# Kernel tuning notes

Hardware: AMD Instinct MI355X
Metric: run time of the kernel (lower is better)

## Reference

```python
import jax, jax.numpy as jnp
import numpy as np

ARRAY_SIZE = 128   # crossbar rows
CBITS = 4          # psum ADC bits
LEV = 2 ** (CBITS - 1)
ALPHA = ARRAY_SIZE / LEV   # psum quant step
EPS = 1e-5

# ---- binary activation / weight quant with STE (hardtanh grad) ----
@jax.custom_vjp
def ste_sign(x):
    return jnp.where(x >= 0, 1.0, -1.0).astype(x.dtype)

def _sign_fwd(x):
    return ste_sign(x), x

def _sign_bwd(x, g):
    return (g * (jnp.abs(x) <= 1.0).astype(g.dtype),)

ste_sign.defvjp(_sign_fwd, _sign_bwd)

# ---- psum (partial-sum) quantization: cbits-level ADC over each crossbar array ----
@jax.custom_vjp
def psum_quant(p):
    return jnp.clip(jnp.round(p / ALPHA), -LEV, LEV - 1) * ALPHA

def _pq_fwd(p):
    return psum_quant(p), p

def _pq_bwd(p, g):
    return (g * (jnp.abs(p) <= ARRAY_SIZE).astype(g.dtype),)

psum_quant.defvjp(_pq_fwd, _pq_bwd)

# ---- layers ----
def bn(x, p):
    g, b, m, v = p  # each [C]
    sh = (1, -1) + (1,) * (x.ndim - 2)
    return (x - m.reshape(sh)) * (g.reshape(sh) / jnp.sqrt(v.reshape(sh) + EPS)) + b.reshape(sh)

def maxpool2(x):
    return jax.lax.reduce_window(x, -jnp.inf, jax.lax.max, (1, 1, 2, 2), (1, 1, 2, 2), 'VALID')

def conv_same(x, w):
    return jax.lax.conv_general_dilated(x, w, (1, 1), 'SAME')

def psum_conv(x, w):
    # crossbar-mapped conv: input channels split into groups of arraySize//(kh*kw),
    # each group conv'd separately, psum-quantized (ADC), then accumulated.
    O, Cin, kh, kw = w.shape
    chunk = max(1, ARRAY_SIZE // (kh * kw))
    G = -(-Cin // chunk)
    pad = G * chunk - Cin
    xp = jnp.pad(x, ((0, 0), (0, pad), (0, 0), (0, 0)))
    wp = jnp.pad(w, ((0, 0), (0, pad), (0, 0), (0, 0)))
    B, _, H, W = x.shape
    xg = xp.reshape(B, G, chunk, H, W).transpose(1, 0, 2, 3, 4)   # [G,B,c,H,W]
    wg = wp.reshape(O, G, chunk, kh, kw).transpose(1, 0, 2, 3, 4)  # [G,O,c,kh,kw]
    ps = jax.vmap(conv_same)(xg, wg)                               # [G,B,O,H,W]
    return psum_quant(ps).sum(0)

def psum_linear(x, w):
    # x [B,D], w [O,D]; D divisible by ARRAY_SIZE
    B, D = x.shape
    O = w.shape[0]
    G = D // ARRAY_SIZE
    ps = jnp.einsum('bgc,ogc->gbo', x.reshape(B, G, ARRAY_SIZE), w.reshape(O, G, ARRAY_SIZE))
    return psum_quant(ps).sum(0)


def setup_inputs() -> dict:
    key = jax.random.key(0)
    ks = iter(jax.random.split(key, 64))
    def nrm(shape, s=0.05):
        return jax.random.normal(next(ks), shape, jnp.float32) * s
    def bnp(C):
        return jnp.stack([jax.random.uniform(next(ks), (C,), jnp.float32) + 0.5,
                          nrm((C,), 0.1), nrm((C,), 0.1),
                          jax.random.uniform(next(ks), (C,), jnp.float32) + 0.5])
    return dict(
        x=jax.random.normal(next(ks), (64, 3, 32, 32), jnp.float32),
        conv0_w=nrm((128, 3, 3, 3)), bn0=bnp(128),
        w1=nrm((128, 128, 3, 3)), bn1=bnp(128),
        w2=nrm((256, 128, 3, 3)), bn2=bnp(256),
        w3=nrm((256, 256, 3, 3)), bn3=bnp(256),
        w4=nrm((512, 256, 3, 3)), bn4=bnp(512),
        w5=nrm((512, 512, 3, 3)), bn5=bnp(512),
        fc1_w=nrm((1024, 8192)), bnf1=bnp(1024),
        fc2_w=nrm((1024, 1024)), bnf2=bnp(1024),
        out_w=nrm((10, 1024)), out_b=nrm((10,)), bnout=bnp(10),
    )


def reference(x, conv0_w, bn0, w1, bn1, w2, bn2, w3, bn3, w4, bn4, w5, bn5,
              fc1_w, bnf1, fc2_w, bnf2, out_w, out_b, bnout):
    h = conv_same(x, conv0_w)                       # full-precision first conv
    h = ste_sign(bn(h, bn0))
    h = psum_conv(h, ste_sign(w1)); h = maxpool2(h); h = ste_sign(bn(h, bn1))
    h = psum_conv(h, ste_sign(w2)); h = ste_sign(bn(h, bn2))
    h = psum_conv(h, ste_sign(w3)); h = maxpool2(h); h = ste_sign(bn(h, bn3))
    h = psum_conv(h, ste_sign(w4)); h = ste_sign(bn(h, bn4))
    h = psum_conv(h, ste_sign(w5)); h = maxpool2(h); h = ste_sign(bn(h, bn5))
    h = h.reshape(h.shape[0], -1)                   # [B, 8192]
    h = ste_sign(bn(psum_linear(h, ste_sign(fc1_w)), bnf1))
    h = bn(psum_linear(h, ste_sign(fc2_w)), bnf2)   # abits=32 -> identity nonlinear
    h = h @ out_w.T + out_b
    return bn(h, bnout)
```

## Files before the change

### kernel.cpp

```cpp
#include <hip/hip_runtime.h>
#include <cstdint>
#include <cstddef>

using bf16x8 = __attribute__((ext_vector_type(8))) short;
using f32x4  = __attribute__((ext_vector_type(4))) float;
using u32x4  = __attribute__((ext_vector_type(4))) unsigned int;

#define DI __device__ __forceinline__

DI float pq3(float a) {
    return fminf(rintf(a), 7.f);
}
DI float pq16(float ps) {
    return fminf(rintf(ps * 0.0625f), 7.f) * 16.f;
}

DI float bnv(float x, float g, float b, float m, float v) {
    return (x - m) * (g / sqrtf(v + 1e-5f)) + b;
}

DI unsigned short sgn_bf16(float v) {
    return (v >= 0.f) ? (unsigned short)0x3F80 : (unsigned short)0xBF80;
}

__global__ __launch_bounds__(256)
void k_conv0(const float* __restrict__ x, const float* __restrict__ w,
             const float* __restrict__ bnp, unsigned short* __restrict__ out) {
    __shared__ float sX[3][3][36];
    const int b = blockIdx.x >> 5, y = blockIdx.x & 31;
    const int tid = threadIdx.x;
    const int o = tid & 127, xc = tid >> 7;

    for (int i = tid; i < 3 * 3 * 36; i += 256) {
        int col = i % 36, rr = (i / 36) % 3, c = i / 108;
        int gy = y + rr - 1, gx = col - 1;
        float v = 0.f;
        if ((unsigned)gy < 32u && (unsigned)gx < 32u)
            v = x[((b * 3 + c) * 32 + gy) * 32 + gx];
        sX[c][rr][col] = v;
    }
    float wr[27];
    const float* wp = w + o * 27;
    #pragma unroll
    for (int t = 0; t < 27; ++t) wr[t] = wp[t];
    __syncthreads();

    const float bg = bnp[o], bb = bnp[128 + o], bm = bnp[256 + o], bv = bnp[384 + o];
    unsigned short* op = out + ((size_t)(b * 32 + y) * 32) * 128 + o;

    #pragma unroll
    for (int q = 0; q < 4; ++q) {
        float acc0 = 0.f, acc1 = 0.f, acc2 = 0.f, acc3 = 0.f;
        const int X0 = xc * 16 + q * 4;
        #pragma unroll
        for (int c = 0; c < 3; ++c)
            #pragma unroll
            for (int ky = 0; ky < 3; ++ky) {
                float xv0 = sX[c][ky][X0 + 0], xv1 = sX[c][ky][X0 + 1];
                float xv2 = sX[c][ky][X0 + 2], xv3 = sX[c][ky][X0 + 3];
                float xv4 = sX[c][ky][X0 + 4], xv5 = sX[c][ky][X0 + 5];
                float w0 = wr[c * 9 + ky * 3 + 0];
                float w1 = wr[c * 9 + ky * 3 + 1];
                float w2 = wr[c * 9 + ky * 3 + 2];
                acc0 += xv0 * w0 + xv1 * w1 + xv2 * w2;
                acc1 += xv1 * w0 + xv2 * w1 + xv3 * w2;
                acc2 += xv2 * w0 + xv3 * w1 + xv4 * w2;
                acc3 += xv3 * w0 + xv4 * w1 + xv5 * w2;
            }
        op[(size_t)(X0 + 0) * 128] = sgn_bf16(bnv(acc0, bg, bb, bm, bv));
        op[(size_t)(X0 + 1) * 128] = sgn_bf16(bnv(acc1, bg, bb, bm, bv));
        op[(size_t)(X0 + 2) * 128] = sgn_bf16(bnv(acc2, bg, bb, bm, bv));
        op[(size_t)(X0 + 3) * 128] = sgn_bf16(bnv(acc3, bg, bb, bm, bv));
    }
}

__global__ __launch_bounds__(256)
void k_pack_w2(const float* __restrict__ w, unsigned short* __restrict__ wpk,
               int Cin, int O, int G) {
    int idx = blockIdx.x * 256 + threadIdx.x;
    if (idx >= G * O * 160) return;
    int c8 = idx & 7;
    int o  = (idx >> 3) % O;
    int r2 = (idx >> 3) / O;
    int chdw = r2 & 1, tap = (r2 >> 1) % 10, g = r2 / 20;
    int c = chdw * 8 + c8, cg = g * 14 + c;
    unsigned short v = 0;
    if (tap < 9 && c < 14 && cg < Cin)
        v = (w[((size_t)o * Cin + cg) * 9 + tap] >= 0.f) ? (unsigned short)0x3D80
                                                         : (unsigned short)0xBD80;
    wpk[idx] = v;
}

template <int H, int W, int Cin, int O, int G, int RH, int RW, int POOLMODE>
__global__ __launch_bounds__(256)
void k_conv_mfma(const unsigned int* __restrict__ act,
                 const char* __restrict__ wpk2,
                 const float* __restrict__ bnp,
                 unsigned short* __restrict__ outa,
                 unsigned short* __restrict__ a5p,
                 const unsigned int* __restrict__ zbuf) {
    constexpr int SH = RH + 2, SW = RW + 2;
    constexpr int MS = RH * RW / 16;
    constexpr int NREGX = W / RW;
    constexpr int SLOT8 = SH * SW * 8;
    constexpr int NST = (SLOT8 + 255) / 256;
    static_assert(MS == 4, "2x2 decomposition needs MS==4");
    static_assert(POOLMODE != 1 || RW == 16, "pool mode 1 needs RW=16");
    static_assert(POOLMODE != 2 || RW == 8, "pool mode 2 needs 8x8");

    __shared__ __align__(16) unsigned int sA[SH * SW * 12];

    const int tid  = threadIdx.x;
    const int regY = (int)blockIdx.x / NREGX, regX = (int)blockIdx.x % NREGX;
    const int o0   = blockIdx.y * 64;
    const int b    = blockIdx.z;

    const int lane = tid & 63, wv = tid >> 6;
    const int n  = lane & 15;
    const int kb = lane >> 4;
    const int hb = kb >> 1, ch = kb & 1;
    const int mp = wv & 1;
    const int oh = wv >> 1;

    const unsigned int* sptr[NST];
    int sdst[NST];
    #pragma unroll
    for (int it = 0; it < NST; ++it) {
        int i = it * 256 + tid;
        sdst[it] = -1;
        if (i < SLOT8) {
            int cp = i & 7, slot = i >> 3;
            int yy = slot / SW, xx = slot - yy * SW;
            int gy = regY * RH + yy - 1, gx = regX * RW + xx - 1;
            sdst[it] = slot * 12 + (((cp >> 2) + slot) % 3) * 4 + (cp & 3);
            sptr[it] = ((unsigned)gy < (unsigned)H && (unsigned)gx < (unsigned)W)
                     ? act + ((size_t)(b * H + gy) * W + gx) * (Cin / 2) + cp
                     : zbuf + cp;
        }
    }

    int offMS[2][5];
    #pragma unroll
    for (int j = 0; j < 2; ++j) {
        int p = (2 * mp + j) * 16 + n;
        int y = p / RW, x = p % RW;
        #pragma unroll
        for (int s = 0; s < 5; ++s) {
            int t = 2 * s + hb;
            int slotT = (t <= 8) ? ((y + t / 3) * SW + (x + t % 3)) : (y * SW + x);
            offMS[j][s] = slotT * 48 + ((ch + slotT) % 3) * 16;
        }
    }

    float tot[2][2][4];
    #pragma unroll
    for (int j = 0; j < 2; ++j)
        #pragma unroll
        for (int hf = 0; hf < 2; ++hf)
            #pragma unroll
            for (int r = 0; r < 4; ++r) tot[j][hf][r] = 0.f;

    const char* wl = wpk2 + (size_t)(o0 + oh * 32 + n) * 16 + (size_t)ch * (O * 16);

    #pragma unroll 1
    for (int g = 0; g < G; ++g) {
        #pragma unroll
        for (int it = 0; it < NST; ++it)
            if (sdst[it] >= 0) {
                sA[sdst[it]] = *sptr[it];
                sptr[it] += 7;
            }
        bf16x8 bq[2][5];
        #pragma unroll
        for (int s = 0; s < 5; ++s) {
            const char* wt = wl + (size_t)(2 * s + hb) * (2 * O * 16);
            bq[0][s] = *(const bf16x8*)(wt);
            bq[1][s] = *(const bf16x8*)(wt + 256);
        }
        wl += (size_t)20 * O * 16;
        __syncthreads();

        const char* sAc = (const char*)sA;
        #pragma unroll
        for (int j = 0; j < 2; ++j) {
            f32x4 a0 = {0.f, 0.f, 0.f, 0.f}, a1 = {0.f, 0.f, 0.f, 0.f};
            #pragma unroll
            for (int s = 0; s < 5; ++s) {
                bf16x8 af = *(const bf16x8*)(sAc + offMS[j][s]);
                a0 = __builtin_amdgcn_mfma_f32_16x16x32_bf16(af, bq[0][s], a0, 0, 0, 0);
                a1 = __builtin_amdgcn_mfma_f32_16x16x32_bf16(af, bq[1][s], a1, 0, 0, 0);
            }
            #pragma unroll
            for (int r = 0; r < 4; ++r) {
                tot[j][0][r] += pq3(a0[r]);
                tot[j][1][r] += pq3(a1[r]);
            }
        }
        __syncthreads();
    }

    #pragma unroll
    for (int hf = 0; hf < 2; ++hf) {
        const int oc = o0 + oh * 32 + hf * 16 + n;
        const float bg = bnp[oc], bb = bnp[O + oc], bm = bnp[2 * O + oc], bvr = bnp[3 * O + oc];

        if constexpr (POOLMODE == 0) {
            #pragma unroll
            for (int j = 0; j < 2; ++j)
                #pragma unroll
                for (int r = 0; r < 4; ++r) {
                    int p = (2 * mp + j) * 16 + 4 * kb + r;
                    int y = regY * RH + p / RW, x = regX * RW + p % RW;
                    float val = bnv(16.f * tot[j][hf][r], bg, bb, bm, bvr);
                    outa[(((size_t)b * H + y) * W + x) * O + oc] = sgn_bf16(val);
                }
        } else if constexpr (POOLMODE == 1) {
            #pragma unroll
            for (int q = 0; q < 2; ++q) {
                float v = fmaxf(fmaxf(tot[0][hf][2 * q], tot[0][hf][2 * q + 1]),
                                fmaxf(tot[1][hf][2 * q], tot[1][hf][2 * q + 1]));
                float val = bnv(16.f * v, bg, bb, bm, bvr);
                int py = regY * (RH / 2) + mp, px = regX * (RW / 2) + 2 * kb + q;
                outa[(((size_t)b * (H / 2) + py) * (W / 2) + px) * O + oc] = sgn_bf16(val);
            }
        } else {
            #pragma unroll
            for (int j = 0; j < 2; ++j)
                #pragma unroll
                for (int q = 0; q < 2; ++q) {
                    float h = fmaxf(tot[j][hf][2 * q], tot[j][hf][2 * q + 1]);
                    float o2 = __shfl_xor(h, 32);
                    float v = fmaxf(h, o2);
                    if (hb == 0) {
                        float val = bnv(16.f * v, bg, bb, bm, bvr);
                        int d = oc * 16 + (2 * mp + j) * 4 + 2 * ch + q;
                        a5p[((size_t)(d >> 3) * 64 + b) * 8 + (d & 7)] = sgn_bf16(val);
                    }
                }
        }
    }
}

template <int D, int GPB>
__global__ __launch_bounds__(256)
void k_fc_mfma(const unsigned short* __restrict__ bpk, const float* __restrict__ w,
               float* __restrict__ accg) {
    const int lane = threadIdx.x & 63, wv = threadIdx.x >> 6;
    const int n = lane & 15, kb = lane >> 4;
    const int orow = blockIdx.x * 64 + wv * 16 + n;
    const int g0 = blockIdx.y * GPB;

    float tot[4][4];
    #pragma unroll
    for (int s = 0; s < 4; ++s)
        #pragma unroll
        for (int r = 0; r < 4; ++r) tot[s][r] = 0.f;

    #pragma unroll 1
    for (int g = 0; g < GPB; ++g) {
        const int kbase = (g0 + g) * 128;
        f32x4 a0 = {0,0,0,0}, a1 = {0,0,0,0}, a2 = {0,0,0,0}, a3 = {0,0,0,0};
        #pragma unroll
        for (int s = 0; s < 4; ++s) {
            const int k0 = kbase + s * 32 + kb * 8;
            const float* wp = w + (size_t)orow * D + k0;
            float4 wlo = *(const float4*)wp;
            float4 whi = *(const float4*)(wp + 4);
            bf16x8 af;
            af[0] = (short)sgn_bf16(wlo.x); af[1] = (short)sgn_bf16(wlo.y);
            af[2] = (short)sgn_bf16(wlo.z); af[3] = (short)sgn_bf16(wlo.w);
            af[4] = (short)sgn_bf16(whi.x); af[5] = (short)sgn_bf16(whi.y);
            af[6] = (short)sgn_bf16(whi.z); af[7] = (short)sgn_bf16(whi.w);
            const unsigned short* bp = bpk + (size_t)(k0 >> 3) * 512;
            bf16x8 b0 = *(const bf16x8*)(bp + (n +  0) * 8);
            bf16x8 b1 = *(const bf16x8*)(bp + (n + 16) * 8);
            bf16x8 b2 = *(const bf16x8*)(bp + (n + 32) * 8);
            bf16x8 b3 = *(const bf16x8*)(bp + (n + 48) * 8);
            a0 = __builtin_amdgcn_mfma_f32_16x16x32_bf16(af, b0, a0, 0, 0, 0);
            a1 = __builtin_amdgcn_mfma_f32_16x16x32_bf16(af, b1, a1, 0, 0, 0);
            a2 = __builtin_amdgcn_mfma_f32_16x16x32_bf16(af, b2, a2, 0, 0, 0);
            a3 = __builtin_amdgcn_mfma_f32_16x16x32_bf16(af, b3, a3, 0, 0, 0);
        }
        #pragma unroll
        for (int r = 0; r < 4; ++r) {
            tot[0][r] += pq16(a0[r]); tot[1][r] += pq16(a1[r]);
            tot[2][r] += pq16(a2[r]); tot[3][r] += pq16(a3[r]);
        }
    }
    const int od = blockIdx.x * 64 + wv * 16 + kb * 4;
    #pragma unroll
    for (int s = 0; s < 4; ++s)
        #pragma unroll
        for (int r = 0; r < 4; ++r)
            atomicAdd(&accg[(size_t)(od + r) * 64 + s * 16 + n], tot[s][r]);
}

template <bool SIGN>
__global__ __launch_bounds__(256)
void k_fc_ep(const float* __restrict__ accg, const float* __restrict__ bnp,
             unsigned short* __restrict__ packed, float* __restrict__ h2, int O) {
    int idx = blockIdx.x * 256 + threadIdx.x;
    int b = idx & 63, o = idx >> 6;
    float val = bnv(accg[idx], bnp[o], bnp[O + o], bnp[2 * O + o], bnp[3 * O + o]);
    if (SIGN) packed[((size_t)(o >> 3) * 64 + b) * 8 + (o & 7)] = sgn_bf16(val);
    else      h2[(size_t)b * 1024 + o] = val;
}

__global__ __launch_bounds__(64)
void k_out(const float* __restrict__ h2, const float* __restrict__ ow,
           const float* __restrict__ ob, const float* __restrict__ bnp,
           float* __restrict__ out) {
    int b = blockIdx.x / 10, o = blockIdx.x % 10;
    int lane = threadIdx.x;
    float acc = 0.f;
    #pragma unroll
    for (int i = 0; i < 16; ++i) {
        int k = i * 64 + lane;
        acc += h2[b * 1024 + k] * ow[o * 1024 + k];
    }
    #pragma unroll
    for (int off = 32; off; off >>= 1) acc += __shfl_xor(acc, off);
    if (lane == 0)
        out[b * 10 + o] = bnv(acc + ob[o], bnp[o], bnp[10 + o], bnp[20 + o], bnp[30 + o]);
}

extern "C" void kernel_launch(void* const* d_in, const int* in_sizes, int n_in,
                              void* d_out, int out_size, void* d_ws, size_t ws_size,
                              hipStream_t stream) {
    const float* x     = (const float*)d_in[0];
    const float* w0    = (const float*)d_in[1];
    const float* bn0   = (const float*)d_in[2];
    const float* w1    = (const float*)d_in[3];
    const float* bn1   = (const float*)d_in[4];
    const float* w2    = (const float*)d_in[5];
    const float* bn2   = (const float*)d_in[6];
    const float* w3    = (const float*)d_in[7];
    const float* bn3   = (const float*)d_in[8];
    const float* w4    = (const float*)d_in[9];
    const float* bn4   = (const float*)d_in[10];
    const float* w5    = (const float*)d_in[11];
    const float* bn5   = (const float*)d_in[12];
    const float* fc1w  = (const float*)d_in[13];
    const float* bnf1  = (const float*)d_in[14];
    const float* fc2w  = (const float*)d_in[15];
    const float* bnf2  = (const float*)d_in[16];
    const float* outw  = (const float*)d_in[17];
    const float* outb  = (const float*)d_in[18];
    const float* bnout = (const float*)d_in[19];

    char* ws = (char*)d_ws;
    unsigned short* actA  = (unsigned short*)(ws);
    unsigned short* actB  = (unsigned short*)(ws + 16777216);
    unsigned short* wpk   = (unsigned short*)(ws + 20971520);
    unsigned short* a5p   = (unsigned short*)(ws + 27262976);
    unsigned short* a6p   = (unsigned short*)(ws + 28311552);
    float*          h1acc = (float*)(ws + 28442624);
    float*          h2acc = (float*)(ws + 28704768);
    float*          h2    = (float*)(ws + 28966912);
    unsigned int*   zbuf  = (unsigned int*)(ws + 29229056);

    const unsigned int* actA32 = (const unsigned int*)actA;
    const unsigned int* actB32 = (const unsigned int*)actB;
    const char* wpkc = (const char*)wpk;

    hipMemsetAsync(h1acc, 0, 262144, stream);
    hipMemsetAsync(h2acc, 0, 262144, stream);
    hipMemsetAsync(zbuf, 0, 4096, stream);

    k_conv0<<<dim3(2048), dim3(256), 0, stream>>>(x, w0, bn0, actA);

    k_pack_w2<<<dim3(800), dim3(256), 0, stream>>>(w1, wpk, 128, 128, 10);
    k_conv_mfma<32, 32, 128, 128, 10, 4, 16, 1>
        <<<dim3(16, 2, 64), dim3(256), 0, stream>>>(actA32, wpkc, bn1, actB, nullptr, zbuf);

    k_pack_w2<<<dim3(1600), dim3(256), 0, stream>>>(w2, wpk, 128, 256, 10);
    k_conv_mfma<16, 16, 128, 256, 10, 4, 16, 0>
        <<<dim3(4, 4, 64), dim3(256), 0, stream>>>(actB32, wpkc, bn2, actA, nullptr, zbuf);

    k_pack_w2<<<dim3(3040), dim3(256), 0, stream>>>(w3, wpk, 256, 256, 19);
    k_conv_mfma<16, 16, 256, 256, 19, 4, 16, 1>
        <<<dim3(4, 4, 64), dim3(256), 0, stream>>>(actA32, wpkc, bn3, actB, nullptr, zbuf);

    k_pack_w2<<<dim3(6080), dim3(256), 0, stream>>>(w4, wpk, 256, 512, 19);
    k_conv_mfma<8, 8, 256, 512, 19, 8, 8, 0>
        <<<dim3(1, 8, 64), dim3(256), 0, stream>>>(actB32, wpkc, bn4, actA, nullptr, zbuf);

    k_pack_w2<<<dim3(11840), dim3(256), 0, stream>>>(w5, wpk, 512, 512, 37);
    k_conv_mfma<8, 8, 512, 512, 37, 8, 8, 2>
        <<<dim3(1, 8, 64), dim3(256), 0, stream>>>(actA32, wpkc, bn5, nullptr, a5p, zbuf);

    k_fc_mfma<8192, 1><<<dim3(16, 64), dim3(256), 0, stream>>>(a5p, fc1w, h1acc);
    k_fc_ep<true><<<dim3(256), dim3(256), 0, stream>>>(h1acc, bnf1, a6p, nullptr, 1024);
    k_fc_mfma<1024, 1><<<dim3(16, 8), dim3(256), 0, stream>>>(a6p, fc2w, h2acc);
    k_fc_ep<false><<<dim3(256), dim3(256), 0, stream>>>(h2acc, bnf2, nullptr, h2, 1024);
    k_out<<<dim3(640), dim3(64), 0, stream>>>(h2, outw, outb, bnout, (float*)d_out);
}
```

Baseline: 269.2 us.

## Switch crossbar conv MFMA from 16x16x32 to 32x32x16 tiles with tap-wise K

Rewrites the binary conv inner loop so each wave computes a 32-pixel by 32-channel tile with 32x32x16 bf16 MFMAs, one per 3x3 tap, instead of pairs of 16x16x32 MFMAs over packed tap pairs. This drops the padding tenth tap, so there are fewer MFMA slots per group. Weight fragments are now loaded inside the compute loop rather than before the barrier. The epilogue is remapped to the 32x32 accumulator layout for the plain, 2x2-pool and flattened-pool output modes. The risk is higher accumulator register pressure and longer MFMA latency chains, which two alternating accumulators only partly hide.

```diff
diff --git a/kernel.cpp b/kernel.cpp
--- a/kernel.cpp
+++ b/kernel.cpp
@@ -4,6 +4,7 @@
 
 using bf16x8 = __attribute__((ext_vector_type(8))) short;
 using f32x4  = __attribute__((ext_vector_type(4))) float;
+using f32x16 = __attribute__((ext_vector_type(16))) float;
 using u32x4  = __attribute__((ext_vector_type(4))) unsigned int;
 
 #define DI __device__ __forceinline__
@@ -100,11 +101,10 @@
                  unsigned short* __restrict__ a5p,
                  const unsigned int* __restrict__ zbuf) {
     constexpr int SH = RH + 2, SW = RW + 2;
-    constexpr int MS = RH * RW / 16;
     constexpr int NREGX = W / RW;
     constexpr int SLOT8 = SH * SW * 8;
     constexpr int NST = (SLOT8 + 255) / 256;
-    static_assert(MS == 4, "2x2 decomposition needs MS==4");
+    static_assert(RH * RW == 64, "tile must be 64 px");
     static_assert(POOLMODE != 1 || RW == 16, "pool mode 1 needs RW=16");
     static_assert(POOLMODE != 2 || RW == 8, "pool mode 2 needs 8x8");
 
@@ -116,11 +116,10 @@
     const int b    = blockIdx.z;
 
     const int lane = tid & 63, wv = tid >> 6;
-    const int n  = lane & 15;
-    const int kb = lane >> 4;
-    const int hb = kb >> 1, ch = kb & 1;
-    const int mp = wv & 1;
-    const int oh = wv >> 1;
+    const int ph   = wv & 1;
+    const int ohl  = wv >> 1;
+    const int l31  = lane & 31;
+    const int chdw = lane >> 5;
 
     const unsigned int* sptr[NST];
     int sdst[NST];
@@ -139,28 +138,19 @@
         }
     }
 
-    int offMS[2][5];
-    #pragma unroll
-    for (int j = 0; j < 2; ++j) {
-        int p = (2 * mp + j) * 16 + n;
-        int y = p / RW, x = p % RW;
-        #pragma unroll
-        for (int s = 0; s < 5; ++s) {
-            int t = 2 * s + hb;
-            int slotT = (t <= 8) ? ((y + t / 3) * SW + (x + t % 3)) : (y * SW + x);
-            offMS[j][s] = slotT * 48 + ((ch + slotT) % 3) * 16;
-        }
-    }
-
-    float tot[2][2][4];
-    #pragma unroll
-    for (int j = 0; j < 2; ++j)
-        #pragma unroll
-        for (int hf = 0; hf < 2; ++hf)
-            #pragma unroll
-            for (int r = 0; r < 4; ++r) tot[j][hf][r] = 0.f;
-
-    const char* wl = wpk2 + (size_t)(o0 + oh * 32 + n) * 16 + (size_t)ch * (O * 16);
+    const int py = (ph * 32 + l31) / RW, px = (ph * 32 + l31) % RW;
+    int offA[9];
+    #pragma unroll
+    for (int t = 0; t < 9; ++t) {
+        int slotT = (py + t / 3) * SW + (px + t % 3);
+        offA[t] = slotT * 48 + ((chdw + slotT) % 3) * 16;
+    }
+
+    float tot[16];
+    #pragma unroll
+    for (int r = 0; r < 16; ++r) tot[r] = 0.f;
+
+    const char* wb = wpk2 + ((size_t)chdw * O + o0 + ohl * 32 + l31) * 16;
 
     #pragma unroll 1
     for (int g = 0; g < G; ++g) {
@@ -170,74 +160,62 @@
                 sA[sdst[it]] = *sptr[it];
                 sptr[it] += 7;
             }
-        bf16x8 bq[2][5];
-        #pragma unroll
-        for (int s = 0; s < 5; ++s) {
-            const char* wt = wl + (size_t)(2 * s + hb) * (2 * O * 16);
-            bq[0][s] = *(const bf16x8*)(wt);
-            bq[1][s] = *(const bf16x8*)(wt + 256);
-        }
-        wl += (size_t)20 * O * 16;
         __syncthreads();
 
         const char* sAc = (const char*)sA;
-        #pragma unroll
-        for (int j = 0; j < 2; ++j) {
-            f32x4 a0 = {0.f, 0.f, 0.f, 0.f}, a1 = {0.f, 0.f, 0.f, 0.f};
+        const char* wg = wb + (size_t)g * (20 * O * 16);
+        f32x16 ac0 = {0.f}, ac1 = {0.f};
+        #pragma unroll
+        for (int t = 0; t < 9; ++t) {
+            bf16x8 bf = *(const bf16x8*)(wg + (size_t)t * (2 * O * 16));
+            bf16x8 af = *(const bf16x8*)(sAc + offA[t]);
+            if (t & 1) ac1 = __builtin_amdgcn_mfma_f32_32x32x16_bf16(af, bf, ac1, 0, 0, 0);
+            else       ac0 = __builtin_amdgcn_mfma_f32_32x32x16_bf16(af, bf, ac0, 0, 0, 0);
+        }
+        #pragma unroll
+        for (int r = 0; r < 16; ++r) tot[r] += pq3(ac0[r] + ac1[r]);
+        __syncthreads();
+    }
+
+    const int oc = o0 + ohl * 32 + l31;
+    const float bg = bnp[oc], bb = bnp[O + oc], bm = bnp[2 * O + oc], bvr = bnp[3 * O + oc];
+
+    if constexpr (POOLMODE == 0) {
+        #pragma unroll
+        for (int r = 0; r < 16; ++r) {
+            int m = (r & 3) + 8 * (r >> 2) + 4 * chdw;
+            int p = ph * 32 + m;
+            int y = regY * RH + p / RW, x = regX * RW + p % RW;
+            float val = bnv(16.f * tot[r], bg, bb, bm, bvr);
+            outa[(((size_t)b * H + y) * W + x) * O + oc] = sgn_bf16(val);
+        }
+    } else if constexpr (POOLMODE == 1) {
+        #pragma unroll
+        for (int i2 = 0; i2 < 2; ++i2)
             #pragma unroll
-            for (int s = 0; s < 5; ++s) {
-                bf16x8 af = *(const bf16x8*)(sAc + offMS[j][s]);
-                a0 = __builtin_amdgcn_mfma_f32_16x16x32_bf16(af, bq[0][s], a0, 0, 0, 0);
-                a1 = __builtin_amdgcn_mfma_f32_16x16x32_bf16(af, bq[1][s], a1, 0, 0, 0);
+            for (int i1 = 0; i1 < 2; ++i1) {
+                int r0 = 2 * i1 + 4 * i2;
+                float v = fmaxf(fmaxf(tot[r0], tot[r0 + 1]),
+                                fmaxf(tot[r0 + 8], tot[r0 + 9]));
+                float val = bnv(16.f * v, bg, bb, bm, bvr);
+                int px2 = regX * 8 + i1 + 2 * chdw + 4 * i2;
+                int py2 = regY * 2 + ph;
+                outa[(((size_t)b * (H / 2) + py2) * (W / 2) + px2) * O + oc] = sgn_bf16(val);
             }
+    } else {
+        #pragma unroll
+        for (int i3 = 0; i3 < 2; ++i3)
             #pragma unroll
-            for (int r = 0; r < 4; ++r) {
-                tot[j][0][r] += pq3(a0[r]);
-                tot[j][1][r] += pq3(a1[r]);
+            for (int i1 = 0; i1 < 2; ++i1) {
+                int r0 = 2 * i1 + 8 * i3;
+                float v = fmaxf(fmaxf(tot[r0], tot[r0 + 1]),
+                                fmaxf(tot[r0 + 4], tot[r0 + 5]));
+                float val = bnv(16.f * v, bg, bb, bm, bvr);
+                int x2 = i1 + 2 * chdw;
+                int y2 = ph * 2 + i3;
+                int d = oc * 16 + y2 * 4 + x2;
+                a5p[((size_t)(d >> 3) * 64 + b) * 8 + (d & 7)] = sgn_bf16(val);
             }
-        }
-        __syncthreads();
-    }
-
-    #pragma unroll
-    for (int hf = 0; hf < 2; ++hf) {
-        const int oc = o0 + oh * 32 + hf * 16 + n;
-        const float bg = bnp[oc], bb = bnp[O + oc], bm = bnp[2 * O + oc], bvr = bnp[3 * O + oc];
-
-        if constexpr (POOLMODE == 0) {
-            #pragma unroll
-            for (int j = 0; j < 2; ++j)
-                #pragma unroll
-                for (int r = 0; r < 4; ++r) {
-                    int p = (2 * mp + j) * 16 + 4 * kb + r;
-                    int y = regY * RH + p / RW, x = regX * RW + p % RW;
-                    float val = bnv(16.f * tot[j][hf][r], bg, bb, bm, bvr);
-                    outa[(((size_t)b * H + y) * W + x) * O + oc] = sgn_bf16(val);
-                }
-        } else if constexpr (POOLMODE == 1) {
-            #pragma unroll
-            for (int q = 0; q < 2; ++q) {
-                float v = fmaxf(fmaxf(tot[0][hf][2 * q], tot[0][hf][2 * q + 1]),
-                                fmaxf(tot[1][hf][2 * q], tot[1][hf][2 * q + 1]));
-                float val = bnv(16.f * v, bg, bb, bm, bvr);
-                int py = regY * (RH / 2) + mp, px = regX * (RW / 2) + 2 * kb + q;
-                outa[(((size_t)b * (H / 2) + py) * (W / 2) + px) * O + oc] = sgn_bf16(val);
-            }
-        } else {
-            #pragma unroll
-            for (int j = 0; j < 2; ++j)
-                #pragma unroll
-                for (int q = 0; q < 2; ++q) {
-                    float h = fmaxf(tot[j][hf][2 * q], tot[j][hf][2 * q + 1]);
-                    float o2 = __shfl_xor(h, 32);
-                    float v = fmaxf(h, o2);
-                    if (hb == 0) {
-                        float val = bnv(16.f * v, bg, bb, bm, bvr);
-                        int d = oc * 16 + (2 * mp + j) * 4 + 2 * ch + q;
-                        a5p[((size_t)(d >> 3) * 64 + b) * 8 + (d & 7)] = sgn_bf16(val);
-                    }
-                }
-        }
     }
 }
 
```

Measured after the change: 272.9 us. No clear change (+1.3%).
